# Kernel optimization log

Measured on AMD Instinct MI355X. Metric: run time of the kernel, lower is better.

Reference implementation:

```python
import jax, jax.numpy as jnp
import numpy as np

N, E = 50000, 400000
IN_DIM, HID, OUT = 512, 256, 128


def _lin(key, fan_in, fan_out, bias=True):
    k1, k2 = jax.random.split(key)
    s = 1.0 / np.sqrt(fan_in)
    W = jax.random.uniform(k1, (fan_in, fan_out), minval=-s, maxval=s, dtype=jnp.float32)
    if bias:
        b = jax.random.uniform(k2, (fan_out,), minval=-s, maxval=s, dtype=jnp.float32)
        return W, b
    return W


def setup_inputs() -> dict:
    key = jax.random.key(0)
    ks = jax.random.split(key, 16)
    feature_data = jax.random.normal(ks[0], (N, IN_DIM), dtype=jnp.float32)
    edge_info = jax.random.randint(ks[1], (2, E), 0, N, dtype=jnp.int32)
    W1, b1 = _lin(ks[2], IN_DIM, HID)
    W2, b2 = _lin(ks[3], HID, HID)
    W3, b3 = _lin(ks[4], HID, HID)
    # SAGEConv params: lin_l (aggregated neighbors, with bias), lin_r (root, no bias)
    Wl1, bl1 = _lin(ks[5], HID, HID); Wr1 = _lin(ks[6], HID, HID, bias=False)
    WlH, blH = _lin(ks[7], HID, HID); WrH = _lin(ks[8], HID, HID, bias=False)
    Wl2, bl2 = _lin(ks[9], HID, HID); Wr2 = _lin(ks[10], HID, HID, bias=False)
    Wp1, bp1 = _lin(ks[11], HID, HID)
    Wp2, bp2 = _lin(ks[12], HID, HID)
    Wp3, bp3 = _lin(ks[13], HID, OUT)
    return dict(feature_data=feature_data, edge_info=edge_info,
                W1=W1, b1=b1, W2=W2, b2=b2, W3=W3, b3=b3,
                Wl1=Wl1, bl1=bl1, Wr1=Wr1,
                WlH=WlH, blH=blH, WrH=WrH,
                Wl2=Wl2, bl2=bl2, Wr2=Wr2,
                Wp1=Wp1, bp1=bp1, Wp2=Wp2, bp2=bp2, Wp3=Wp3, bp3=bp3)


def _sage_softmax_conv(x, src, dst, Wl, bl, Wr, n_nodes):
    # messages are source node features
    m = x[src]                                                   # [E, d]
    mx = jax.ops.segment_max(m, dst, num_segments=n_nodes)      # per-dest, per-channel max
    e = jnp.exp(m - mx[dst])                                     # stable softmax numerator
    s = jax.ops.segment_sum(e, dst, num_segments=n_nodes)
    alpha = e / s[dst]                                           # per-dest channel softmax
    aggr = jax.ops.segment_sum(alpha * m, dst, num_segments=n_nodes)  # [N, d]
    return aggr @ Wl + bl + x @ Wr


def reference(feature_data, edge_info,
              W1, b1, W2, b2, W3, b3,
              Wl1, bl1, Wr1, WlH, blH, WrH, Wl2, bl2, Wr2,
              Wp1, bp1, Wp2, bp2, Wp3, bp3):
    n = feature_data.shape[0]
    src, dst = edge_info[0], edge_info[1]
    # eval mode: dropout is identity
    x = jax.nn.relu(feature_data @ W1 + b1)
    x = jax.nn.relu(x @ W2 + b2)
    x = jax.nn.relu(x @ W3 + b3)
    x = jax.nn.relu(_sage_softmax_conv(x, src, dst, Wl1, bl1, Wr1, n))
    x = jax.nn.relu(_sage_softmax_conv(x, src, dst, WlH, blH, WrH, n))
    x = jax.nn.relu(_sage_softmax_conv(x, src, dst, Wl2, bl2, Wr2, n))
    x = jax.nn.relu(x @ Wp1 + bp1)
    x = jax.nn.relu(x @ Wp2 + bp2)
    return jnp.tanh(x @ Wp3 + bp3)
```

## Files before the change

### kernel.cpp

```cpp
#include <hip/hip_runtime.h>
#include <hip/hip_bf16.h>
#include <math.h>

typedef short s8v __attribute__((ext_vector_type(8)));
typedef float f32x4 __attribute__((ext_vector_type(4)));
typedef unsigned u32x4 __attribute__((ext_vector_type(4)));

__device__ __forceinline__ ushort f2bf(float f) {
    __hip_bfloat16 h = __float2bfloat16(f);
    return *reinterpret_cast<ushort*>(&h);
}
__device__ __forceinline__ float bf2f(ushort u) {
    return __uint_as_float(((unsigned)u) << 16);
}
__device__ __forceinline__ unsigned pack_split(float v) {
    ushort h = f2bf(v);
    ushort l = f2bf(v - bf2f(h));
    return ((unsigned)h << 16) | (unsigned)l;
}
__device__ __forceinline__ float unpack_f(unsigned p) {
    return __uint_as_float(p & 0xffff0000u) + __uint_as_float(p << 16);
}
__device__ __forceinline__ void gload16(const void* g, void* l) {
    __builtin_amdgcn_global_load_lds(
        (const __attribute__((address_space(1))) void*)g,
        (__attribute__((address_space(3))) void*)l, 16, 0, 0);
}
__device__ __forceinline__ unsigned lds_addr(const void* p) {
    return (unsigned)(size_t)(const __attribute__((address_space(3))) void*)p;
}
__device__ __forceinline__ void unpack8(const u32x4 p0, const u32x4 p1, s8v& hi, s8v& lo) {
    union { s8v v; unsigned u[4]; } H, L;
    H.u[0] = (p0[0] >> 16) | (p0[1] & 0xffff0000u);
    H.u[1] = (p0[2] >> 16) | (p0[3] & 0xffff0000u);
    H.u[2] = (p1[0] >> 16) | (p1[1] & 0xffff0000u);
    H.u[3] = (p1[2] >> 16) | (p1[3] & 0xffff0000u);
    L.u[0] = (p0[0] & 0xffffu) | (p0[1] << 16);
    L.u[1] = (p0[2] & 0xffffu) | (p0[3] << 16);
    L.u[2] = (p1[0] & 0xffffu) | (p1[1] << 16);
    L.u[3] = (p1[2] & 0xffffu) | (p1[3] << 16);
    hi = H.v; lo = L.v;
}
__device__ __forceinline__ void cvt8(const u32x4 p0, const u32x4 p1, s8v& hi, s8v& lo) {
    union { s8v v; ushort e[8]; } H, L;
    float f[8] = {__uint_as_float(p0[0]), __uint_as_float(p0[1]),
                  __uint_as_float(p0[2]), __uint_as_float(p0[3]),
                  __uint_as_float(p1[0]), __uint_as_float(p1[1]),
                  __uint_as_float(p1[2]), __uint_as_float(p1[3])};
    #pragma unroll
    for (int e = 0; e < 8; ++e) {
        ushort h = f2bf(f[e]);
        H.e[e] = (ushort)h;
        L.e[e] = f2bf(f[e] - bf2f(h));
    }
    hi = H.v; lo = L.v;
}
template<bool AF32>
__device__ __forceinline__ void frag_a(const u32x4 p0, const u32x4 p1, s8v& hi, s8v& lo) {
    if constexpr (AF32) cvt8(p0, p1, hi, lo);
    else                unpack8(p0, p1, hi, lo);
}

#define DSR(dst, addr, OFF) \
    asm volatile("ds_read_b128 %0, %1 offset:" #OFF : "=v"(dst) : "v"(addr))

#define TRI(ah, al, bh, bl, C) \
    C = __builtin_amdgcn_mfma_f32_16x16x32_bf16(ah, bh, C, 0, 0, 0); \
    C = __builtin_amdgcn_mfma_f32_16x16x32_bf16(ah, bl, C, 0, 0, 0); \
    C = __builtin_amdgcn_mfma_f32_16x16x32_bf16(al, bh, C, 0, 0, 0);


__global__ __launch_bounds__(256)
void hist_kernel(const int* __restrict__ dst, int* __restrict__ cnt, int E) {
    int e = blockIdx.x * 256 + threadIdx.x;
    if (e < E) atomicAdd(&cnt[dst[e]], 1);
}

__global__ __launch_bounds__(1024)
void scan_kernel(const int* __restrict__ cnt, int* __restrict__ off, int n) {
    __shared__ int lds[1024];
    int t = threadIdx.x;
    int chunk = (n + 1023) >> 10;
    int begin = t * chunk;
    int end = min(begin + chunk, n);
    if (end < begin) end = begin;
    int s = 0;
    for (int i = begin; i < end; ++i) s += cnt[i];
    lds[t] = s;
    __syncthreads();
    for (int d = 1; d < 1024; d <<= 1) {
        int v = (t >= d) ? lds[t - d] : 0;
        __syncthreads();
        lds[t] += v;
        __syncthreads();
    }
    int pre = (t == 0) ? 0 : lds[t - 1];
    for (int i = begin; i < end; ++i) { off[i] = pre; pre += cnt[i]; }
    if (t == 1023) off[n] = pre;
}

__global__ __launch_bounds__(256)
void scatter_kernel(const int* __restrict__ src, const int* __restrict__ dst,
                    int* __restrict__ cur, const int* __restrict__ off,
                    int* __restrict__ csr, int E) {
    int e = blockIdx.x * 256 + threadIdx.x;
    if (e < E) {
        int d = dst[e];
        int pos = off[d] + atomicAdd(&cur[d], 1);
        csr[pos] = src[e];
    }
}


struct PrepW {
    const float* W[12];
    unsigned* D[12];
    int end[12];
    int stride[12];
    int koff[12];
    int nshift[12];
};

__global__ __launch_bounds__(256)
void prep_weights(PrepW a, int total) {
    int id = blockIdx.x * 256 + threadIdx.x;
    if (id >= total) return;
    int s = 0;
    #pragma unroll
    for (int i = 0; i < 12; ++i) if (id >= a.end[i]) s = i + 1;
    int base = (s == 0) ? 0 : a.end[s - 1];
    int e = id - base;
    int Nmask = (1 << a.nshift[s]) - 1;
    int n = e & Nmask;
    int k = e >> a.nshift[s];
    float w = a.W[s][(size_t)k * (Nmask + 1) + n];
    a.D[s][(size_t)n * a.stride[s] + a.koff[s] + k] = pack_split(w);
}


__global__ __launch_bounds__(256)
void sage_aggr_pk(const unsigned* __restrict__ X, const int* __restrict__ csr,
                  const int* __restrict__ off, unsigned* __restrict__ O, int nN) {
    int node = blockIdx.x * 4 + (threadIdx.x >> 6);
    if (node >= nN) return;
    int c4 = (threadIdx.x & 63) * 4;
    int s0 = off[node], s1 = off[node + 1];
    float m0 = -INFINITY, m1 = -INFINITY, m2 = -INFINITY, m3 = -INFINITY;
    float se0 = 0, se1 = 0, se2 = 0, se3 = 0;
    float sm0 = 0, sm1 = 0, sm2 = 0, sm3 = 0;
#define ONLSTEP(vv, mm, ss, pp) { float nm = fmaxf(mm, vv); float r = __expf(mm - nm); \
    float p = __expf(vv - nm); ss = ss * r + p; pp = pp * r + p * (vv); mm = nm; }
    for (int j = s0; j < s1; ++j) {
        uint4 p = *(const uint4*)(X + (size_t)csr[j] * 256 + c4);
        float v0 = unpack_f(p.x), v1 = unpack_f(p.y), v2 = unpack_f(p.z), v3 = unpack_f(p.w);
        ONLSTEP(v0, m0, se0, sm0) ONLSTEP(v1, m1, se1, sm1)
        ONLSTEP(v2, m2, se2, sm2) ONLSTEP(v3, m3, se3, sm3)
    }
#undef ONLSTEP
    uint4 o;
    o.x = pack_split((s1 > s0) ? sm0 / se0 : 0.f);
    o.y = pack_split((s1 > s0) ? sm1 / se1 : 0.f);
    o.z = pack_split((s1 > s0) ? sm2 / se2 : 0.f);
    o.w = pack_split((s1 > s0) ? sm3 / se3 : 0.f);
    *(uint4*)(O + (size_t)node * 256 + c4) = o;
}


template<int NT1, int NT2, bool AF32, int NB, bool DOTANH>
__global__ __launch_bounds__(512, 2)
void gemm_pipe(const float* __restrict__ A1f, const unsigned* __restrict__ A1,
               const unsigned* __restrict__ A2,
               const unsigned* __restrict__ B,
               const float* __restrict__ bias,
               unsigned* __restrict__ Cpk, float* __restrict__ Cf, int M) {
    constexpr int NT = NT1 + NT2;
    constexpr int KU = NT * 32;
    __shared__ unsigned lds[3][12288];

    const int tid = threadIdx.x;
    const int l = tid & 63;
    const int w = tid >> 6;
    const int wm = w >> 2, wn = w & 3;
    const int li = l & 15, kq = l >> 4;
    const int bm = blockIdx.x * 128;

    const int srow = 8 * w + (l >> 3);
    const int schunk = (l & 7) ^ (l >> 3);

    const unsigned lbase = lds_addr(&lds[0][0]);
    const unsigned swz0 = (unsigned)((((2 * kq)) ^ (li & 7)) * 16);
    const unsigned aoff = (unsigned)((wm * 64 + li) * 128) + swz0;
    const unsigned boff = 16384u + (unsigned)((wn * 64 + li) * 128) + swz0;

    f32x4 acc[4][4];
    #pragma unroll
    for (int i = 0; i < 4; ++i)
        #pragma unroll
        for (int j = 0; j < 4; ++j) acc[i][j] = (f32x4){0.f, 0.f, 0.f, 0.f};

    auto STAGE = [&](int t, int buf) {
        #pragma unroll
        for (int s = 0; s < 2; ++s) {
            int r = 64 * s + srow;
            int gr = bm + r; gr = (gr < M) ? gr : (M - 1);
            const void* src;
            if constexpr (AF32) {
                src = A1f + (size_t)gr * KU + t * 32 + schunk * 4;
            } else if constexpr (NT2 > 0) {
                src = (t < NT1) ? (const void*)(A1 + (size_t)gr * (NT1 * 32) + t * 32 + schunk * 4)
                                : (const void*)(A2 + (size_t)gr * (NT2 * 32) + (t - NT1) * 32 + schunk * 4);
            } else {
                src = A1 + (size_t)gr * KU + t * 32 + schunk * 4;
            }
            gload16(src, &lds[buf][s * 2048 + w * 256 + l * 4]);
        }
        #pragma unroll
        for (int s = 0; s < 4; ++s) {
            int n = 64 * s + srow;
            int gn = (n < NB) ? n : (NB - 1);
            const unsigned* src = B + (size_t)gn * KU + t * 32 + schunk * 4;
            gload16(src, &lds[buf][4096 + s * 2048 + w * 256 + l * 4]);
        }
    };

    STAGE(0, 0);
    STAGE(1, 1);

    #pragma unroll
    for (int t = 0; t < NT; ++t) {
        if (t + 1 < NT) asm volatile("s_waitcnt vmcnt(6)" ::: "memory");
        else            asm volatile("s_waitcnt vmcnt(0)" ::: "memory");
        __builtin_amdgcn_s_barrier();

        const int buf = t % 3;
        const unsigned lb = lbase + (unsigned)buf * 49152u;
        unsigned ab = lb + aoff, bb = lb + boff;
        unsigned ab1 = ab ^ 16u, bb1 = bb ^ 16u;

        u32x4 B0, B1, B2, B3, B4, B5, B6, B7;
        u32x4 A0, A1v, A2v, A3, A4, A5, A6, A7;
        DSR(B0, bb, 0);    DSR(B1, bb, 2048);  DSR(B2, bb, 4096);  DSR(B3, bb, 6144);
        DSR(B4, bb1, 0);   DSR(B5, bb1, 2048); DSR(B6, bb1, 4096); DSR(B7, bb1, 6144);
        DSR(A0, ab, 0);    DSR(A1v, ab, 2048); DSR(A2v, ab, 4096); DSR(A3, ab, 6144);
        DSR(A4, ab1, 0);   DSR(A5, ab1, 2048); DSR(A6, ab1, 4096); DSR(A7, ab1, 6144);
        __builtin_amdgcn_sched_barrier(0);

        if (t + 2 < NT) STAGE(t + 2, (t + 2) % 3);
        __builtin_amdgcn_sched_barrier(0);

        asm volatile("s_waitcnt lgkmcnt(0)" ::: "memory");
        __builtin_amdgcn_sched_barrier(0);

        s8v bh0, bl0, bh1, bl1, bh2, bl2, bh3, bl3;
        unpack8(B0, B4, bh0, bl0);
        unpack8(B1, B5, bh1, bl1);
        unpack8(B2, B6, bh2, bl2);
        unpack8(B3, B7, bh3, bl3);

        __builtin_amdgcn_s_setprio(1);
        {
            s8v ah, al;
            frag_a<AF32>(A0, A4, ah, al);
            TRI(ah, al, bh0, bl0, acc[0][0]) TRI(ah, al, bh1, bl1, acc[0][1])
            TRI(ah, al, bh2, bl2, acc[0][2]) TRI(ah, al, bh3, bl3, acc[0][3])
        }
        {
            s8v ah, al;
            frag_a<AF32>(A1v, A5, ah, al);
            TRI(ah, al, bh0, bl0, acc[1][0]) TRI(ah, al, bh1, bl1, acc[1][1])
            TRI(ah, al, bh2, bl2, acc[1][2]) TRI(ah, al, bh3, bl3, acc[1][3])
        }
        {
            s8v ah, al;
            frag_a<AF32>(A2v, A6, ah, al);
            TRI(ah, al, bh0, bl0, acc[2][0]) TRI(ah, al, bh1, bl1, acc[2][1])
            TRI(ah, al, bh2, bl2, acc[2][2]) TRI(ah, al, bh3, bl3, acc[2][3])
        }
        {
            s8v ah, al;
            frag_a<AF32>(A3, A7, ah, al);
            TRI(ah, al, bh0, bl0, acc[3][0]) TRI(ah, al, bh1, bl1, acc[3][1])
            TRI(ah, al, bh2, bl2, acc[3][2]) TRI(ah, al, bh3, bl3, acc[3][3])
        }
        __builtin_amdgcn_s_setprio(0);
    }

    #pragma unroll
    for (int j = 0; j < 4; ++j) {
        int col = wn * 64 + 16 * j + li;
        float b = bias[(col < NB) ? col : 0];
        #pragma unroll
        for (int i = 0; i < 4; ++i) {
            int row0 = bm + wm * 64 + 16 * i + kq * 4;
            #pragma unroll
            for (int r = 0; r < 4; ++r) {
                float v = acc[i][j][r] + b;
                if constexpr (DOTANH) {
                    if (row0 + r < M && col < NB)
                        Cf[(size_t)(row0 + r) * NB + col] = tanhf(v);
                } else {
                    Cpk[(size_t)(row0 + r) * 256 + col] = pack_split(fmaxf(v, 0.f));
                }
            }
        }
    }
}


extern "C" void kernel_launch(void* const* d_in, const int* in_sizes, int n_in,
                              void* d_out, int out_size, void* d_ws, size_t ws_size,
                              hipStream_t stream) {
    const float* feat = (const float*)d_in[0];
    const int* einfo = (const int*)d_in[1];
    const float* b1 = (const float*)d_in[3];
    const float* b2 = (const float*)d_in[5];
    const float* b3 = (const float*)d_in[7];
    const float* bl1 = (const float*)d_in[9];
    const float* blH = (const float*)d_in[12];
    const float* bl2 = (const float*)d_in[15];
    const float* bp1 = (const float*)d_in[18];
    const float* bp2 = (const float*)d_in[20];
    const float* bp3 = (const float*)d_in[22];

    const int IN_DIM = 512;
    const int N = in_sizes[0] / IN_DIM;
    const int E = in_sizes[1] / 2;
    const int* src = einfo;
    const int* dst = einfo + E;
    const int M_pad = ((N + 127) / 128) * 128;
    const size_t PLANE_U = (size_t)M_pad * 256;

    unsigned* P0 = (unsigned*)d_ws;
    unsigned* P1 = P0 + PLANE_U;
    unsigned* P2 = P1 + PLANE_U;
    unsigned* wp = P2 + PLANE_U;

    const int gsz[9] = {131072, 65536, 65536, 131072, 131072, 131072, 65536, 65536, 32768};
    unsigned* G[9];
    {
        unsigned* c = wp;
        for (int i = 0; i < 9; ++i) { G[i] = c; c += gsz[i]; }
        wp = c;
    }

    const int widx[12]   = {2, 4, 6, 8, 10, 11, 13, 14, 16, 17, 19, 21};
    const int wplane[12] = {0, 1, 2, 3, 3, 4, 4, 5, 5, 6, 7, 8};
    const int wstr[12]   = {512, 256, 256, 512, 512, 512, 512, 512, 512, 256, 256, 256};
    const int wkoff[12]  = {0, 0, 0, 0, 256, 0, 256, 0, 256, 0, 0, 0};
    const int wnsh[12]   = {8, 8, 8, 8, 8, 8, 8, 8, 8, 8, 8, 7};
    const int welem[12]  = {131072, 65536, 65536, 65536, 65536, 65536, 65536,
                            65536, 65536, 65536, 65536, 32768};

    PrepW pa;
    int acc_end = 0;
    for (int i = 0; i < 12; ++i) {
        pa.W[i] = (const float*)d_in[widx[i]];
        pa.D[i] = G[wplane[i]];
        pa.stride[i] = wstr[i];
        pa.koff[i] = wkoff[i];
        pa.nshift[i] = wnsh[i];
        acc_end += welem[i];
        pa.end[i] = acc_end;
    }

    int* ioff = (int*)wp;
    int* icnt = ioff + (N + 1);
    int* icur = icnt + N;
    int* csr = icur + N;

    hipMemsetAsync(icnt, 0, (size_t)N * sizeof(int), stream);
    hipMemsetAsync(icur, 0, (size_t)N * sizeof(int), stream);
    hist_kernel<<<(E + 255) / 256, 256, 0, stream>>>(dst, icnt, E);
    scan_kernel<<<1, 1024, 0, stream>>>(icnt, ioff, N);
    scatter_kernel<<<(E + 255) / 256, 256, 0, stream>>>(src, dst, icur, ioff, csr, E);
    prep_weights<<<(acc_end + 255) / 256, 256, 0, stream>>>(pa, acc_end);

    const int GB = M_pad / 128;
    const int GA = (N + 3) / 4;

    gemm_pipe<16, 0, true, 256, false><<<GB, 512, 0, stream>>>(
        feat, nullptr, nullptr, G[0], b1, P0, nullptr, N);
    gemm_pipe<8, 0, false, 256, false><<<GB, 512, 0, stream>>>(
        nullptr, P0, nullptr, G[1], b2, P1, nullptr, N);
    gemm_pipe<8, 0, false, 256, false><<<GB, 512, 0, stream>>>(
        nullptr, P1, nullptr, G[2], b3, P0, nullptr, N);

    sage_aggr_pk<<<GA, 256, 0, stream>>>(P0, csr, ioff, P1, N);
    gemm_pipe<8, 8, false, 256, false><<<GB, 512, 0, stream>>>(
        nullptr, P1, P0, G[3], bl1, P2, nullptr, N);

    sage_aggr_pk<<<GA, 256, 0, stream>>>(P2, csr, ioff, P1, N);
    gemm_pipe<8, 8, false, 256, false><<<GB, 512, 0, stream>>>(
        nullptr, P1, P2, G[4], blH, P0, nullptr, N);

    sage_aggr_pk<<<GA, 256, 0, stream>>>(P0, csr, ioff, P1, N);
    gemm_pipe<8, 8, false, 256, false><<<GB, 512, 0, stream>>>(
        nullptr, P1, P0, G[5], bl2, P2, nullptr, N);

    gemm_pipe<8, 0, false, 256, false><<<GB, 512, 0, stream>>>(
        nullptr, P2, nullptr, G[6], bp1, P0, nullptr, N);
    gemm_pipe<8, 0, false, 256, false><<<GB, 512, 0, stream>>>(
        nullptr, P0, nullptr, G[7], bp2, P1, nullptr, N);
    gemm_pipe<8, 0, false, 128, true><<<GB, 512, 0, stream>>>(
        nullptr, P1, nullptr, G[8], bp3, nullptr, (float*)d_out, N);
}
```

Measured before the change: 742.6 us.

## Parallelize CSR offset scan and interleave A-fragment LDS reads with MFMA

Replaces the single-block serial-chunk prefix scan over node degrees with a three-kernel multi-block scan (partial block sums, a wave-level scan of block sums, final per-block scan) that uses vectorized int4 loads. Separately, the GEMM inner loop now issues A-fragment LDS reads incrementally, waiting only for the fragment needed next so that later reads overlap with MFMA work. It also aligns workspace sub-buffers to 4 ints for the vector loads. The new scan adds two extra launches and scan_top assumes at most 64 blocks, which holds for N=50000 but not for much larger graphs.

```diff
diff --git a/kernel.cpp b/kernel.cpp
--- a/kernel.cpp
+++ b/kernel.cpp
@@ -76,27 +76,71 @@
     if (e < E) atomicAdd(&cnt[dst[e]], 1);
 }
 
-__global__ __launch_bounds__(1024)
-void scan_kernel(const int* __restrict__ cnt, int* __restrict__ off, int n) {
-    __shared__ int lds[1024];
-    int t = threadIdx.x;
-    int chunk = (n + 1023) >> 10;
-    int begin = t * chunk;
-    int end = min(begin + chunk, n);
-    if (end < begin) end = begin;
-    int s = 0;
-    for (int i = begin; i < end; ++i) s += cnt[i];
-    lds[t] = s;
+__global__ __launch_bounds__(256)
+void scan_part(const int* __restrict__ cnt, int* __restrict__ bsum, int n) {
+    __shared__ int s[256];
+    int b = blockIdx.x, t = threadIdx.x;
+    int i0 = b * 1024 + t * 4;
+    int v = 0;
+    if (i0 + 3 < n) {
+        int4 q = *(const int4*)(cnt + i0);
+        v = q.x + q.y + q.z + q.w;
+    } else {
+        for (int i = 0; i < 4; ++i) if (i0 + i < n) v += cnt[i0 + i];
+    }
+    s[t] = v;
     __syncthreads();
-    for (int d = 1; d < 1024; d <<= 1) {
-        int v = (t >= d) ? lds[t - d] : 0;
+    for (int d = 128; d > 0; d >>= 1) {
+        if (t < d) s[t] += s[t + d];
         __syncthreads();
-        lds[t] += v;
+    }
+    if (t == 0) bsum[b] = s[0];
+}
+
+__global__ __launch_bounds__(64)
+void scan_top(int* __restrict__ bsum, int nb) {
+    int l = threadIdx.x;
+    int own = (l < nb) ? bsum[l] : 0;
+    int v = own;
+    #pragma unroll
+    for (int d = 1; d < 64; d <<= 1) {
+        int u = __shfl_up(v, d, 64);
+        if (l >= d) v += u;
+    }
+    if (l < nb) bsum[l] = v - own;
+}
+
+__global__ __launch_bounds__(256)
+void scan_final(const int* __restrict__ cnt, const int* __restrict__ bsum,
+                int* __restrict__ off, int n, int E) {
+    __shared__ int s[256];
+    int b = blockIdx.x, t = threadIdx.x;
+    int i0 = b * 1024 + t * 4;
+    int v0 = 0, v1 = 0, v2 = 0, v3 = 0;
+    if (i0 + 3 < n) {
+        int4 q = *(const int4*)(cnt + i0);
+        v0 = q.x; v1 = q.y; v2 = q.z; v3 = q.w;
+    } else {
+        if (i0     < n) v0 = cnt[i0];
+        if (i0 + 1 < n) v1 = cnt[i0 + 1];
+        if (i0 + 2 < n) v2 = cnt[i0 + 2];
+        if (i0 + 3 < n) v3 = cnt[i0 + 3];
+    }
+    int tsum = v0 + v1 + v2 + v3;
+    s[t] = tsum;
+    __syncthreads();
+    for (int d = 1; d < 256; d <<= 1) {
+        int u = (t >= d) ? s[t - d] : 0;
         __syncthreads();
-    }
-    int pre = (t == 0) ? 0 : lds[t - 1];
-    for (int i = begin; i < end; ++i) { off[i] = pre; pre += cnt[i]; }
-    if (t == 1023) off[n] = pre;
+        s[t] += u;
+        __syncthreads();
+    }
+    int excl = s[t] - tsum + bsum[b];
+    if (i0     < n) off[i0]     = excl;
+    if (i0 + 1 < n) off[i0 + 1] = excl + v0;
+    if (i0 + 2 < n) off[i0 + 2] = excl + v0 + v1;
+    if (i0 + 3 < n) off[i0 + 3] = excl + v0 + v1 + v2;
+    if (b == 0 && t == 0) off[n] = E;
 }
 
 __global__ __launch_bounds__(256)
@@ -238,17 +282,17 @@
         unsigned ab1 = ab ^ 16u, bb1 = bb ^ 16u;
 
         u32x4 B0, B1, B2, B3, B4, B5, B6, B7;
-        u32x4 A0, A1v, A2v, A3, A4, A5, A6, A7;
+        u32x4 A0, A4, A1v, A5, A2v, A6, A3, A7;
         DSR(B0, bb, 0);    DSR(B1, bb, 2048);  DSR(B2, bb, 4096);  DSR(B3, bb, 6144);
         DSR(B4, bb1, 0);   DSR(B5, bb1, 2048); DSR(B6, bb1, 4096); DSR(B7, bb1, 6144);
-        DSR(A0, ab, 0);    DSR(A1v, ab, 2048); DSR(A2v, ab, 4096); DSR(A3, ab, 6144);
-        DSR(A4, ab1, 0);   DSR(A5, ab1, 2048); DSR(A6, ab1, 4096); DSR(A7, ab1, 6144);
+        DSR(A0, ab, 0);    DSR(A4, ab1, 0);
         __builtin_amdgcn_sched_barrier(0);
 
         if (t + 2 < NT) STAGE(t + 2, (t + 2) % 3);
         __builtin_amdgcn_sched_barrier(0);
 
-        asm volatile("s_waitcnt lgkmcnt(0)" ::: "memory");
+        DSR(A1v, ab, 2048); DSR(A5, ab1, 2048);
+        asm volatile("s_waitcnt lgkmcnt(2)" ::: "memory");
         __builtin_amdgcn_sched_barrier(0);
 
         s8v bh0, bl0, bh1, bl1, bh2, bl2, bh3, bl3;
@@ -264,18 +308,28 @@
             TRI(ah, al, bh0, bl0, acc[0][0]) TRI(ah, al, bh1, bl1, acc[0][1])
             TRI(ah, al, bh2, bl2, acc[0][2]) TRI(ah, al, bh3, bl3, acc[0][3])
         }
+        __builtin_amdgcn_sched_barrier(0);
+        DSR(A2v, ab, 4096); DSR(A6, ab1, 4096);
+        asm volatile("s_waitcnt lgkmcnt(2)" ::: "memory");
+        __builtin_amdgcn_sched_barrier(0);
         {
             s8v ah, al;
             frag_a<AF32>(A1v, A5, ah, al);
             TRI(ah, al, bh0, bl0, acc[1][0]) TRI(ah, al, bh1, bl1, acc[1][1])
             TRI(ah, al, bh2, bl2, acc[1][2]) TRI(ah, al, bh3, bl3, acc[1][3])
         }
+        __builtin_amdgcn_sched_barrier(0);
+        DSR(A3, ab, 6144); DSR(A7, ab1, 6144);
+        asm volatile("s_waitcnt lgkmcnt(2)" ::: "memory");
+        __builtin_amdgcn_sched_barrier(0);
         {
             s8v ah, al;
             frag_a<AF32>(A2v, A6, ah, al);
             TRI(ah, al, bh0, bl0, acc[2][0]) TRI(ah, al, bh1, bl1, acc[2][1])
             TRI(ah, al, bh2, bl2, acc[2][2]) TRI(ah, al, bh3, bl3, acc[2][3])
         }
+        asm volatile("s_waitcnt lgkmcnt(0)" ::: "memory");
+        __builtin_amdgcn_sched_barrier(0);
         {
             s8v ah, al;
             frag_a<AF32>(A3, A7, ah, al);
@@ -364,14 +418,19 @@
     }
 
     int* ioff = (int*)wp;
-    int* icnt = ioff + (N + 1);
-    int* icur = icnt + N;
-    int* csr = icur + N;
+    int* icnt = ioff + ((N + 1 + 3) & ~3);
+    int* icur = icnt + ((N + 3) & ~3);
+    int* csr  = icur + ((N + 3) & ~3);
+    int* bsum = csr + ((E + 3) & ~3);
+
+    const int NBLK = (N + 1023) / 1024;
 
     hipMemsetAsync(icnt, 0, (size_t)N * sizeof(int), stream);
     hipMemsetAsync(icur, 0, (size_t)N * sizeof(int), stream);
     hist_kernel<<<(E + 255) / 256, 256, 0, stream>>>(dst, icnt, E);
-    scan_kernel<<<1, 1024, 0, stream>>>(icnt, ioff, N);
+    scan_part<<<NBLK, 256, 0, stream>>>(icnt, bsum, N);
+    scan_top<<<1, 64, 0, stream>>>(bsum, NBLK);
+    scan_final<<<NBLK, 256, 0, stream>>>(icnt, bsum, ioff, N, E);
     scatter_kernel<<<(E + 255) / 256, 256, 0, stream>>>(src, dst, icur, ioff, csr, E);
     prep_weights<<<(acc_end + 255) / 256, 256, 0, stream>>>(pa, acc_end);
 
```

Result: faster. 652.1 us (-12.2%).
